# Kernel tuning notes

Hardware: AMD Instinct MI355X
Metric: run time of the kernel (lower is better)

Reference implementation:

```python
import jax, jax.numpy as jnp
import numpy as np
from jax import lax

B, T, R = 64, 32, 49
LOCAL, QVEC, EMB, HID, VOCAB = 1024, 512, 256, 512, 10000
START_IDX = 1


def setup_inputs() -> dict:
    key = jax.random.key(0)
    ks = jax.random.split(key, 20)
    s = lambda k, shape, scale=0.02: jax.random.normal(k, shape, dtype=jnp.float32) * scale
    return {
        "image_local_features": jax.random.normal(ks[0], (B, R, LOCAL), dtype=jnp.float32),
        "image_global_features": jax.random.normal(ks[1], (B, 2 * LOCAL), dtype=jnp.float32),
        "question_vectors": jax.random.normal(ks[2], (B, QVEC), dtype=jnp.float32),
        "answers": jax.random.randint(ks[3], (B, T), 0, VOCAB),
        "emb": s(ks[4], (VOCAB, EMB), 1.0),
        "W_g2o": s(ks[5], (HID, 2 * LOCAL)),
        "b_g2o": jnp.zeros((HID,), jnp.float32),
        "W_h": s(ks[6], (HID, QVEC)),
        "W_c": s(ks[7], (HID, QVEC)),
        "W_ih": s(ks[8], (4 * HID, EMB + HID)),
        "W_hh": s(ks[9], (4 * HID, HID)),
        "b_ih": jnp.zeros((4 * HID,), jnp.float32),
        "b_hh": jnp.zeros((4 * HID,), jnp.float32),
        "W_attn": s(ks[10], (HID, LOCAL)),
        "W_u": s(ks[11], (HID, LOCAL + HID)),
        "b_u": jnp.zeros((HID,), jnp.float32),
        "W_vocab": s(ks[12], (VOCAB, HID)),
        "b_vocab": jnp.zeros((VOCAB,), jnp.float32),
    }


def reference(image_local_features, image_global_features, question_vectors, answers,
              emb, W_g2o, b_g2o, W_h, W_c, W_ih, W_hh, b_ih, b_hh,
              W_attn, W_u, b_u, W_vocab, b_vocab):
    batch, max_len = answers.shape
    # initial decoder inputs / states
    y0 = jnp.broadcast_to(emb[START_IDX], (batch, emb.shape[1]))          # [B,E]
    o0 = image_global_features @ W_g2o.T + b_g2o                          # [B,H]
    h0 = question_vectors @ W_h.T                                         # [B,H]
    c0 = question_vectors @ W_c.T                                         # [B,H]
    # teacher forcing: input at step t is answers[t-1] (start token at t=0)
    ans_emb = emb[answers]                                                # [B,T,E]
    y_seq = jnp.concatenate([y0[:, None, :], ans_emb[:, :-1, :]], axis=1) # [B,T,E]
    y_seq = jnp.swapaxes(y_seq, 0, 1)                                     # [T,B,E]
    # precompute attention projection of local features (loop-invariant)
    attn_proj = jnp.einsum('brf,hf->brh', image_local_features, W_attn)   # [B,R,H]

    def step(carry, y_t):
        h, c, o = carry
        x = jnp.concatenate([y_t, o], axis=1)                             # [B,E+H]
        gates = x @ W_ih.T + b_ih + h @ W_hh.T + b_hh                     # [B,4H]
        i_g, f_g, g_g, o_g = jnp.split(gates, 4, axis=1)
        c = jax.nn.sigmoid(f_g) * c + jax.nn.sigmoid(i_g) * jnp.tanh(g_g)
        h = jax.nn.sigmoid(o_g) * jnp.tanh(c)
        e = jnp.einsum('brh,bh->br', attn_proj, h)                        # [B,R]
        att = jax.nn.softmax(e, axis=-1)
        a = jnp.einsum('brf,br->bf', image_local_features, att)           # [B,F]
        u = jnp.concatenate([a, h], axis=1)                               # [B,F+H]
        o = jnp.tanh(u @ W_u.T + b_u)                                     # dropout_prob=0 -> identity
        logits = o @ W_vocab.T + b_vocab                                  # [B,V]
        return (h, c, o), logits

    _, logits = lax.scan(step, (h0, c0, o0), y_seq)                       # [T,B,V]
    return jnp.swapaxes(logits, 0, 1)                                     # [B,T,V]
```

## Files before the change

### kernel.cpp

```cpp
#include <hip/hip_runtime.h>

#define DI __device__ __forceinline__

typedef float f32x4 __attribute__((ext_vector_type(4)));
typedef __bf16 bf16x8 __attribute__((ext_vector_type(8)));
typedef __bf16 bf16x4 __attribute__((ext_vector_type(4)));

static DI f32x4 mfma_bf16(bf16x8 a, bf16x8 b, f32x4 c) {
    return __builtin_amdgcn_mfma_f32_16x16x32_bf16(a, b, c, 0, 0, 0);
}
static DI bf16x8 ldb8(const __bf16* p) { return *(const bf16x8*)p; }
static DI float sigf(float x) { return 1.0f / (1.0f + expf(-x)); }

static DI void stc_u32(void* p, unsigned v) {
    __hip_atomic_store((unsigned*)p, v, __ATOMIC_RELAXED, __HIP_MEMORY_SCOPE_AGENT);
}
static DI void stc_u64(void* p, unsigned long long v) {
    __hip_atomic_store((unsigned long long*)p, v, __ATOMIC_RELAXED, __HIP_MEMORY_SCOPE_AGENT);
}
static DI unsigned ldc_u32(const void* p) {
    return __hip_atomic_load((const unsigned*)p, __ATOMIC_RELAXED, __HIP_MEMORY_SCOPE_AGENT);
}

#define GRID_BLKS 64

static DI void garrive(unsigned* F, int blk, unsigned tgt) {
    __syncthreads();
    if (threadIdx.x == 0)
        __hip_atomic_store(&F[blk], tgt, __ATOMIC_RELAXED, __HIP_MEMORY_SCOPE_AGENT);
}
static DI void gwait_all(unsigned* F, unsigned tgt) {
    if (threadIdx.x < 64) {
        for (;;) {
            unsigned f = __hip_atomic_load(&F[threadIdx.x], __ATOMIC_RELAXED,
                                           __HIP_MEMORY_SCOPE_AGENT);
            if (__all(f >= tgt)) break;
            __builtin_amdgcn_s_sleep(1);
        }
    }
    __syncthreads();
}

__global__ void convert_kernel(
    const float* Wih, const float* Whh,
    const float* bih, const float* bhh, const float* Wu,
    const float* emb, const int* answers,
    __bf16* WGo, float* biasg, __bf16* WhTo, __bf16* Yo)
{
    int z = blockIdx.z;
    int stride = gridDim.x * blockDim.x;
    int tid0 = blockIdx.x * blockDim.x + threadIdx.x;
    if (z == 0) {
        const int N = 2048 * 1280;
        for (int i = tid0; i < N; i += stride) {
            int n = i / 1280, k = i - n * 1280;
            int r = (n & 3) * 512 + (n >> 2);
            float val = (k < 768) ? Wih[r * 768 + k] : Whh[r * 512 + (k - 768)];
            WGo[i] = (__bf16)val;
        }
        for (int n = tid0; n < 2048; n += stride) {
            int r = (n & 3) * 512 + (n >> 2);
            biasg[n] = bih[r] + bhh[r];
        }
    } else if (z == 1) {
        const int N = 512 * 512;
        for (int i = tid0; i < N; i += stride) {
            int k = i >> 9, u = i & 511;
            WhTo[i] = (__bf16)Wu[(size_t)u * 1536 + 1024 + k];
        }
    } else {
        const int N = 32 * 64 * 256;
        for (int i = tid0; i < N; i += stride) {
            int t = i >> 14;
            int b = (i >> 8) & 63;
            int e = i & 255;
            int tok = (t == 0) ? 1 : answers[b * 32 + (t - 1)];
            Yo[i] = (__bf16)emb[tok * 256 + e];
        }
    }
}

__global__ void init_kernel(
    const float* q, const float* g,
    const float* Wh, const float* Wc, const float* Wg2o, const float* bg2o,
    __bf16* h0b, float* c0f, __bf16* o0b)
{
    int z = blockIdx.z;
    const float* A; const float* B; int K;
    if (z == 0)      { A = q; B = Wh;   K = 512; }
    else if (z == 1) { A = q; B = Wc;   K = 512; }
    else             { A = g; B = Wg2o; K = 2048; }
    int n0 = blockIdx.x * 64, m0 = blockIdx.y * 16;
    __shared__ float As[32][16];
    __shared__ float Bs[32][64];
    int tid = threadIdx.x;
    int n = tid & 63, tyq = tid >> 6;
    float acc[4] = {0.f, 0.f, 0.f, 0.f};
    for (int k0 = 0; k0 < K; k0 += 32) {
        {
            int idx = tid * 2, row = idx >> 5, kk = idx & 31;
            const float* ar = A + (m0 + row) * K + k0 + kk;
            As[kk][row] = ar[0];
            As[kk + 1][row] = ar[1];
        }
        {
            int row = tid >> 2, kk = (tid & 3) * 8;
            const float* br = B + (n0 + row) * K + k0 + kk;
            float4 v0 = *(const float4*)br;
            float4 v1 = *(const float4*)(br + 4);
            Bs[kk + 0][row] = v0.x; Bs[kk + 1][row] = v0.y;
            Bs[kk + 2][row] = v0.z; Bs[kk + 3][row] = v0.w;
            Bs[kk + 4][row] = v1.x; Bs[kk + 5][row] = v1.y;
            Bs[kk + 6][row] = v1.z; Bs[kk + 7][row] = v1.w;
        }
        __syncthreads();
        #pragma unroll
        for (int k = 0; k < 32; k++) {
            float4 a = *(const float4*)&As[k][tyq * 4];
            float b = Bs[k][n];
            acc[0] += a.x * b; acc[1] += a.y * b; acc[2] += a.z * b; acc[3] += a.w * b;
        }
        __syncthreads();
    }
    int ng = n0 + n;
    #pragma unroll
    for (int i = 0; i < 4; i++) {
        int m = m0 + tyq * 4 + i;
        float v = acc[i];
        if (z == 0)      { h0b[m * 512 + ng] = (__bf16)v; }
        else if (z == 1) { c0f[m * 512 + ng] = v; }
        else             { o0b[m * 512 + ng] = (__bf16)(v + bg2o[ng]); }
    }
}

__global__ __launch_bounds__(256) void attnproj_kernel(
    const float* Af, const float* Bf, int ldb, __bf16* APo)
{
    __shared__ __bf16 As[64][72];
    __shared__ __bf16 Bs[64][72];
    int tid = threadIdx.x;
    int m0 = blockIdx.x * 64, n0 = blockIdx.y * 64;
    int w = tid >> 6, lane = tid & 63, row16 = lane & 15, kg = lane >> 4;
    f32x4 acc[4] = {};
    for (int k0 = 0; k0 < 1024; k0 += 64) {
        int r = tid >> 2, col = (tid & 3) * 16;
        const float* ap = Af + (size_t)(m0 + r) * 1024 + k0 + col;
        const float* bp = Bf + (size_t)(n0 + r) * ldb + k0 + col;
        bf16x8 va0, va1, vb0, vb1;
        #pragma unroll
        for (int u = 0; u < 8; u++) {
            va0[u] = (__bf16)ap[u]; va1[u] = (__bf16)ap[u + 8];
            vb0[u] = (__bf16)bp[u]; vb1[u] = (__bf16)bp[u + 8];
        }
        *(bf16x8*)&As[r][col] = va0; *(bf16x8*)&As[r][col + 8] = va1;
        *(bf16x8*)&Bs[r][col] = vb0; *(bf16x8*)&Bs[r][col + 8] = vb1;
        __syncthreads();
        #pragma unroll
        for (int kt = 0; kt < 2; kt++) {
            bf16x8 af = *(const bf16x8*)&As[w * 16 + row16][kt * 32 + kg * 8];
            #pragma unroll
            for (int j = 0; j < 4; j++) {
                bf16x8 bfv = *(const bf16x8*)&Bs[j * 16 + row16][kt * 32 + kg * 8];
                acc[j] = mfma_bf16(af, bfv, acc[j]);
            }
        }
        __syncthreads();
    }
    #pragma unroll
    for (int j = 0; j < 4; j++)
        #pragma unroll
        for (int r = 0; r < 4; r++)
            APo[(size_t)(m0 + w * 16 + kg * 4 + r) * 512 + n0 + j * 16 + row16] =
                (__bf16)acc[j][r];
}

__global__ __launch_bounds__(256, 1) void loop_kernel(
    const __bf16* Yall, const __bf16* WG, const float* BG,
    const __bf16* WhT, const float* bu,
    const __bf16* APb, const __bf16* LUb, const float* CF0,
    __bf16* OS, __bf16* HS, __bf16* CHP, unsigned* FLA, unsigned* FLB)
{
    __shared__ float S[64][34];
    __shared__ float Cs[64][8];
    __shared__ float Hs[64][8];
    __shared__ __bf16 Ws[8][512];
    __shared__ __bf16 WGs[32 * 1280];
    __shared__ float BGs[32];
    __shared__ float esh[64];
    __shared__ float ash[64];
    int tid = threadIdx.x;
    int blk = blockIdx.x;
    int w = tid >> 6, lane = tid & 63, row16 = lane & 15, kg4 = lane >> 4;
    int n0 = blk * 32;

    for (int i = tid; i < 32 * 160; i += 256) {
        int n = i / 160, g = i % 160;
        bf16x8 v = ldb8(WG + (size_t)(n0 + n) * 1280 + g * 8);
        *(bf16x8*)((char*)WGs + ((n * 2560 + g * 16) ^ ((n & 7) << 4))) = v;
    }
    for (int i = tid; i < 8 * 512; i += 256)
        Ws[i >> 9][i & 511] = WhT[(size_t)(blk * 8 + (i >> 9)) * 512 + (i & 511)];
    if (tid < 32) BGs[tid] = BG[n0 + tid];
    {
        int b = tid >> 2, u0 = (tid & 3) * 2;
        Cs[b][u0]     = CF0[b * 512 + blk * 8 + u0];
        Cs[b][u0 + 1] = CF0[b * 512 + blk * 8 + u0 + 1];
    }
    __syncthreads();
    float wreg[8][4];
    {
        int u0c = (tid & 127) * 4;
        #pragma unroll
        for (int k = 0; k < 8; k++)
            #pragma unroll
            for (int j = 0; j < 4; j++)
                wreg[k][j] = (float)Ws[k][u0c + j];
    }

    for (int t = 0; t < 32; t++) {
        int arow = w * 16 + row16;
        f32x4 acc[2] = {};
        {
            const __bf16* Yt = Yall + t * 16384;
            const __bf16* Hp = HS + t * 32768;
            bf16x8 a_h[16];
            #pragma unroll
            for (int kt = 0; kt < 16; kt++)
                a_h[kt] = ldb8(Hp + arow * 512 + kt * 32 + kg4 * 8);
            asm volatile("" ::: "memory");
            #pragma unroll
            for (int kt = 0; kt < 8; kt++) {
                bf16x8 af = ldb8(Yt + arow * 256 + kt * 32 + kg4 * 8);
                #pragma unroll
                for (int nt = 0; nt < 2; nt++) {
                    int row = nt * 16 + row16;
                    bf16x8 bfv = *(const bf16x8*)((const char*)WGs +
                        ((row * 2560 + kt * 64 + kg4 * 16) ^ ((row & 7) << 4)));
                    acc[nt] = mfma_bf16(af, bfv, acc[nt]);
                }
            }
            #pragma unroll
            for (int kt = 24; kt < 40; kt++) {
                bf16x8 af = a_h[kt - 24];
                #pragma unroll
                for (int nt = 0; nt < 2; nt++) {
                    int row = nt * 16 + row16;
                    bf16x8 bfv = *(const bf16x8*)((const char*)WGs +
                        ((row * 2560 + kt * 64 + kg4 * 16) ^ ((row & 7) << 4)));
                    acc[nt] = mfma_bf16(af, bfv, acc[nt]);
                }
            }
        }
        gwait_all(FLB, (unsigned)t);

        {
            const __bf16* Op = OS + t * 32768;
            bf16x8 a_o[16];
            #pragma unroll
            for (int kt = 0; kt < 16; kt++)
                a_o[kt] = ldb8(Op + arow * 512 + kt * 32 + kg4 * 8);
            asm volatile("" ::: "memory");
            #pragma unroll
            for (int kt = 8; kt < 24; kt++) {
                bf16x8 af = a_o[kt - 8];
                #pragma unroll
                for (int nt = 0; nt < 2; nt++) {
                    int row = nt * 16 + row16;
                    bf16x8 bfv = *(const bf16x8*)((const char*)WGs +
                        ((row * 2560 + kt * 64 + kg4 * 16) ^ ((row & 7) << 4)));
                    acc[nt] = mfma_bf16(af, bfv, acc[nt]);
                }
            }
            #pragma unroll
            for (int nt = 0; nt < 2; nt++)
                #pragma unroll
                for (int r = 0; r < 4; r++)
                    S[w * 16 + kg4 * 4 + r][nt * 16 + row16] = acc[nt][r];
            __syncthreads();
            {
                int b = tid >> 2, u0 = (tid & 3) * 2;
                float h2[2];
                #pragma unroll
                for (int uu = 0; uu < 2; uu++) {
                    int u = u0 + uu;
                    float gi = S[b][u * 4 + 0] + BGs[u * 4 + 0];
                    float gf = S[b][u * 4 + 1] + BGs[u * 4 + 1];
                    float gg = S[b][u * 4 + 2] + BGs[u * 4 + 2];
                    float go = S[b][u * 4 + 3] + BGs[u * 4 + 3];
                    float cp = Cs[b][u];
                    float cn = sigf(gf) * cp + sigf(gi) * tanhf(gg);
                    h2[uu] = sigf(go) * tanhf(cn);
                    Cs[b][u] = cn;
                }
                Hs[b][u0] = h2[0];
                Hs[b][u0 + 1] = h2[1];
                union { __bf16 h[2]; unsigned v; } pk;
                pk.h[0] = (__bf16)h2[0]; pk.h[1] = (__bf16)h2[1];
                stc_u32((unsigned*)(HS + (t + 1) * 32768 + b * 512 + blk * 8 + u0), pk.v);
            }
            __syncthreads();
            {
                __bf16* CHPt = CHP + (size_t)(t & 1) * 2097152;
                int bh = tid >> 7;
                int u0 = (tid & 127) * 4;
                #pragma unroll 4
                for (int bb = 0; bb < 32; bb++) {
                    int b = bh * 32 + bb;
                    float4 hv0 = *(const float4*)&Hs[b][0];
                    float4 hv1 = *(const float4*)&Hs[b][4];
                    float a0 = 0.f, a1 = 0.f, a2 = 0.f, a3 = 0.f;
                    a0 += hv0.x * wreg[0][0]; a1 += hv0.x * wreg[0][1];
                    a2 += hv0.x * wreg[0][2]; a3 += hv0.x * wreg[0][3];
                    a0 += hv0.y * wreg[1][0]; a1 += hv0.y * wreg[1][1];
                    a2 += hv0.y * wreg[1][2]; a3 += hv0.y * wreg[1][3];
                    a0 += hv0.z * wreg[2][0]; a1 += hv0.z * wreg[2][1];
                    a2 += hv0.z * wreg[2][2]; a3 += hv0.z * wreg[2][3];
                    a0 += hv0.w * wreg[3][0]; a1 += hv0.w * wreg[3][1];
                    a2 += hv0.w * wreg[3][2]; a3 += hv0.w * wreg[3][3];
                    a0 += hv1.x * wreg[4][0]; a1 += hv1.x * wreg[4][1];
                    a2 += hv1.x * wreg[4][2]; a3 += hv1.x * wreg[4][3];
                    a0 += hv1.y * wreg[5][0]; a1 += hv1.y * wreg[5][1];
                    a2 += hv1.y * wreg[5][2]; a3 += hv1.y * wreg[5][3];
                    a0 += hv1.z * wreg[6][0]; a1 += hv1.z * wreg[6][1];
                    a2 += hv1.z * wreg[6][2]; a3 += hv1.z * wreg[6][3];
                    a0 += hv1.w * wreg[7][0]; a1 += hv1.w * wreg[7][1];
                    a2 += hv1.w * wreg[7][2]; a3 += hv1.w * wreg[7][3];
                    union { __bf16 h[4]; unsigned long long q; } pk;
                    pk.h[0] = (__bf16)a0; pk.h[1] = (__bf16)a1;
                    pk.h[2] = (__bf16)a2; pk.h[3] = (__bf16)a3;
                    stc_u64(CHPt + ((size_t)blk * 64 + b) * 512 + u0, pk.q);
                }
            }
        }
        garrive(FLA, blk, (unsigned)(t + 1));
        gwait_all(FLA, (unsigned)(t + 1));

        {
            int b = blk;
            const __bf16* hb = HS + (size_t)(t + 1) * 32768 + b * 512;
            const __bf16* CHPt = CHP + (size_t)(t & 1) * 2097152;
            bf16x8 h8 = ldb8(hb + lane * 8);
            unsigned cv[64];
            {
                const __bf16* cp = CHPt + (size_t)b * 512 + tid * 2;
                #pragma unroll
                for (int p = 0; p < 64; p++)
                    cv[p] = ldc_u32(cp + (size_t)p * 32768);
            }
            asm volatile("" ::: "memory");
            for (int r = w; r < 49; r += 4) {
                bf16x8 ap8 = ldb8(APb + (size_t)(b * 49 + r) * 512 + lane * 8);
                float s = 0.f;
                #pragma unroll
                for (int u = 0; u < 8; u++) s += (float)ap8[u] * (float)h8[u];
                #pragma unroll
                for (int off = 32; off > 0; off >>= 1) s += __shfl_xor(s, off);
                if (lane == 0) esh[r] = s;
            }
            __syncthreads();
            if (tid < 64) {
                float v = (tid < 49) ? esh[tid] : -3.0e38f;
                float mx = v;
                #pragma unroll
                for (int off = 32; off > 0; off >>= 1) mx = fmaxf(mx, __shfl_xor(mx, off));
                float ex = (tid < 49) ? expf(v - mx) : 0.0f;
                float sm = ex;
                #pragma unroll
                for (int off = 32; off > 0; off >>= 1) sm += __shfl_xor(sm, off);
                if (tid < 49) ash[tid] = ex / sm;
            }
            float oh0, oh1;
            {
                float s00 = 0.f, s01 = 0.f, s10 = 0.f, s11 = 0.f;
                float s20 = 0.f, s21 = 0.f, s30 = 0.f, s31 = 0.f;
                #pragma unroll
                for (int p = 0; p < 64; p += 4) {
                    union { unsigned u; __bf16 h[2]; } c0, c1, c2, c3;
                    c0.u = cv[p]; c1.u = cv[p + 1]; c2.u = cv[p + 2]; c3.u = cv[p + 3];
                    s00 += (float)c0.h[0]; s01 += (float)c0.h[1];
                    s10 += (float)c1.h[0]; s11 += (float)c1.h[1];
                    s20 += (float)c2.h[0]; s21 += (float)c2.h[1];
                    s30 += (float)c3.h[0]; s31 += (float)c3.h[1];
                }
                oh0 = (s00 + s10) + (s20 + s30);
                oh1 = (s01 + s11) + (s21 + s31);
            }
            __syncthreads();
            float oa0 = 0.f, oa1 = 0.f, ob0 = 0.f, ob1 = 0.f;
            {
                const __bf16* lu = LUb + (size_t)b * 49 * 512 + tid * 2;
                #pragma unroll 8
                for (int r = 0; r < 48; r += 2) {
                    float wt0 = ash[r], wt1 = ash[r + 1];
                    union { unsigned u; __bf16 h[2]; } c0, c1;
                    c0.u = *(const unsigned*)(lu + (size_t)r * 512);
                    c1.u = *(const unsigned*)(lu + (size_t)(r + 1) * 512);
                    oa0 += wt0 * (float)c0.h[0]; oa1 += wt0 * (float)c0.h[1];
                    ob0 += wt1 * (float)c1.h[0]; ob1 += wt1 * (float)c1.h[1];
                }
                float wt = ash[48];
                union { unsigned u; __bf16 h[2]; } c;
                c.u = *(const unsigned*)(lu + (size_t)48 * 512);
                oa0 += wt * (float)c.h[0]; oa1 += wt * (float)c.h[1];
                oa0 += ob0; oa1 += ob1;
            }
            int u = tid * 2;
            float o0v = tanhf(oh0 + oa0 + bu[u]);
            float o1v = tanhf(oh1 + oa1 + bu[u + 1]);
            union { __bf16 h[2]; unsigned v; } pk;
            pk.h[0] = (__bf16)o0v; pk.h[1] = (__bf16)o1v;
            stc_u32((unsigned*)(OS + (size_t)(t + 1) * 32768 + b * 512 + u), pk.v);
        }
        garrive(FLB, blk, (unsigned)(t + 1));
    }
}

__global__ __launch_bounds__(256) void vocab_kernel(
    const __bf16* A, const float* Wv, const float* bv, float* out)
{
    __shared__ __bf16 As[128][72];
    __shared__ __bf16 Bs[128][72];
    int tid = threadIdx.x;
    int m0 = blockIdx.x * 128;
    int n0 = blockIdx.y * 128;
    int w = tid >> 6, lane = tid & 63, row16 = lane & 15, kg = lane >> 4;
    int mw = (w & 1) * 64, nw = (w >> 1) * 64;
    f32x4 acc[4][4] = {};
    for (int k0 = 0; k0 < 512; k0 += 64) {
        #pragma unroll
        for (int q = 0; q < 2; q++) {
            int c = q * 256 + tid;
            int r = c >> 2, col = (c & 3) * 16;
            bf16x8 v0 = ldb8(A + (size_t)(m0 + r) * 512 + k0 + col);
            bf16x8 v1 = ldb8(A + (size_t)(m0 + r) * 512 + k0 + col + 8);
            *(bf16x8*)&As[r][col] = v0;
            *(bf16x8*)&As[r][col + 8] = v1;
            bf16x8 u0, u1;
            int nrow = n0 + r;
            if (nrow < 10000) {
                const float* bp = Wv + (size_t)nrow * 512 + k0 + col;
                #pragma unroll
                for (int u = 0; u < 8; u++) {
                    u0[u] = (__bf16)bp[u];
                    u1[u] = (__bf16)bp[u + 8];
                }
            } else {
                u0 = (bf16x8)(__bf16)0.0f;
                u1 = (bf16x8)(__bf16)0.0f;
            }
            *(bf16x8*)&Bs[r][col] = u0;
            *(bf16x8*)&Bs[r][col + 8] = u1;
        }
        __syncthreads();
        #pragma unroll
        for (int kt = 0; kt < 2; kt++) {
            bf16x8 af[4], bfr[4];
            #pragma unroll
            for (int i = 0; i < 4; i++)
                af[i] = *(const bf16x8*)&As[mw + i * 16 + row16][kt * 32 + kg * 8];
            #pragma unroll
            for (int j = 0; j < 4; j++)
                bfr[j] = *(const bf16x8*)&Bs[nw + j * 16 + row16][kt * 32 + kg * 8];
            #pragma unroll
            for (int i = 0; i < 4; i++)
                #pragma unroll
                for (int j = 0; j < 4; j++)
                    acc[i][j] = mfma_bf16(af[i], bfr[j], acc[i][j]);
        }
        __syncthreads();
    }
    #pragma unroll
    for (int j = 0; j < 4; j++) {
        int n = n0 + nw + j * 16 + row16;
        if (n < 10000) {
            float bvn = bv[n];
            #pragma unroll
            for (int i = 0; i < 4; i++) {
                #pragma unroll
                for (int r = 0; r < 4; r++) {
                    int m = m0 + mw + i * 16 + kg * 4 + r;
                    int tt = m >> 6, b = m & 63;
                    out[(size_t)(b * 32 + tt) * 10000 + n] = acc[i][j][r] + bvn;
                }
            }
        }
    }
}

extern "C" void kernel_launch(void* const* d_in, const int* in_sizes, int n_in,
                              void* d_out, int out_size, void* d_ws, size_t ws_size,
                              hipStream_t stream) {
    (void)in_sizes; (void)n_in; (void)out_size; (void)ws_size;
    const float* localf  = (const float*)d_in[0];
    const float* globalf = (const float*)d_in[1];
    const float* qvec    = (const float*)d_in[2];
    const int*   answers = (const int*)d_in[3];
    const float* emb     = (const float*)d_in[4];
    const float* Wg2o    = (const float*)d_in[5];
    const float* bg2o    = (const float*)d_in[6];
    const float* Wh      = (const float*)d_in[7];
    const float* Wc      = (const float*)d_in[8];
    const float* Wih     = (const float*)d_in[9];
    const float* Whh     = (const float*)d_in[10];
    const float* bih     = (const float*)d_in[11];
    const float* bhh     = (const float*)d_in[12];
    const float* Wattn   = (const float*)d_in[13];
    const float* Wu      = (const float*)d_in[14];
    const float* bu      = (const float*)d_in[15];
    const float* Wvocab  = (const float*)d_in[16];
    const float* bvocab  = (const float*)d_in[17];
    float* out = (float*)d_out;

    char* ws = (char*)d_ws;
    __bf16* WG  = (__bf16*)(ws + 0);
    __bf16* WhT = (__bf16*)(ws + 5242880);
    __bf16* Y   = (__bf16*)(ws + 5767168);
    float*  BG  = (float*) (ws + 6815744);
    __bf16* OS  = (__bf16*)(ws + 6823936);
    __bf16* HS  = (__bf16*)(ws + 8986624);
    float*  CF0 = (float*) (ws + 11149312);
    __bf16* APb = (__bf16*)(ws + 11280384);
    __bf16* LUb = (__bf16*)(ws + 14491648);
    __bf16* CHP = (__bf16*)(ws + 17702912);
    unsigned* FLA = (unsigned*)(ws + 26091520);
    unsigned* FLB = (unsigned*)(ws + 26091776);

    hipMemsetAsync(FLA, 0, 512, stream);
    convert_kernel<<<dim3(1024, 1, 3), 256, 0, stream>>>(
        Wih, Whh, bih, bhh, Wu, emb, answers,
        WG, BG, WhT, Y);
    init_kernel<<<dim3(8, 4, 3), 256, 0, stream>>>(
        qvec, globalf, Wh, Wc, Wg2o, bg2o, HS, CF0, OS);
    attnproj_kernel<<<dim3(49, 8), 256, 0, stream>>>(localf, Wattn, 1024, APb);
    attnproj_kernel<<<dim3(49, 8), 256, 0, stream>>>(localf, Wu, 1536, LUb);
    loop_kernel<<<GRID_BLKS, 256, 0, stream>>>(
        Y, WG, BG, WhT, bu, APb, LUb, CF0, OS, HS, CHP, FLA, FLB);
    vocab_kernel<<<dim3(16, 79), 256, 0, stream>>>(OS + 32768, Wvocab, bvocab, out);
}
```

Measured before the change: 1.123 ms.

## Split recurrent loop into LSTM and attention block roles, stage weights in LDS

The persistent loop kernel now launches 128 blocks. Blocks 0-63 compute the LSTM gates and blocks 64-127 each handle one batch row's attention and output projection, handing off through the FLA/FLB flags. The per-batch attention projection and local-feature tables are now cached in shared memory rather than reread from global memory every step. The vocab GEMM is restructured so each block converts one 128-row slice of W_vocab to bf16 once and reuses it across 8 M tiles, and the weight conversion kernel now walks rows. This cuts the per-step global barrier into a producer/consumer pipeline and avoids repeated fp32 weight conversion, at the cost of more LDS per block and more flag polling.

```diff
diff --git a/kernel.cpp b/kernel.cpp
--- a/kernel.cpp
+++ b/kernel.cpp
@@ -22,12 +22,11 @@
     return __hip_atomic_load((const unsigned*)p, __ATOMIC_RELAXED, __HIP_MEMORY_SCOPE_AGENT);
 }
 
-#define GRID_BLKS 64
-
-static DI void garrive(unsigned* F, int blk, unsigned tgt) {
+
+static DI void garrive(unsigned* F, int idx, unsigned tgt) {
     __syncthreads();
     if (threadIdx.x == 0)
-        __hip_atomic_store(&F[blk], tgt, __ATOMIC_RELAXED, __HIP_MEMORY_SCOPE_AGENT);
+        __hip_atomic_store(&F[idx], tgt, __ATOMIC_RELAXED, __HIP_MEMORY_SCOPE_AGENT);
 }
 static DI void gwait_all(unsigned* F, unsigned tgt) {
     if (threadIdx.x < 64) {
@@ -51,14 +50,18 @@
     int stride = gridDim.x * blockDim.x;
     int tid0 = blockIdx.x * blockDim.x + threadIdx.x;
     if (z == 0) {
-        const int N = 2048 * 1280;
-        for (int i = tid0; i < N; i += stride) {
-            int n = i / 1280, k = i - n * 1280;
+        #pragma unroll
+        for (int rr = 0; rr < 2; rr++) {
+            int n = blockIdx.x * 2 + rr;
             int r = (n & 3) * 512 + (n >> 2);
-            float val = (k < 768) ? Wih[r * 768 + k] : Whh[r * 512 + (k - 768)];
-            WGo[i] = (__bf16)val;
-        }
-        for (int n = tid0; n < 2048; n += stride) {
+            const float* sih = Wih + (size_t)r * 768;
+            const float* shh = Whh + (size_t)r * 512;
+            __bf16* dst = WGo + (size_t)n * 1280;
+            for (int k = threadIdx.x; k < 1280; k += 256)
+                dst[k] = (__bf16)((k < 768) ? sih[k] : shh[k - 768]);
+        }
+        if (blockIdx.x < 8) {
+            int n = blockIdx.x * 256 + threadIdx.x;
             int r = (n & 3) * 512 + (n >> 2);
             biasg[n] = bih[r] + bhh[r];
         }
@@ -185,158 +188,172 @@
     __shared__ float Hs[64][8];
     __shared__ __bf16 Ws[8][512];
     __shared__ __bf16 WGs[32 * 1280];
+    __shared__ __bf16 LUs[49 * 512];
     __shared__ float BGs[32];
     __shared__ float esh[64];
     __shared__ float ash[64];
     int tid = threadIdx.x;
     int blk = blockIdx.x;
     int w = tid >> 6, lane = tid & 63, row16 = lane & 15, kg4 = lane >> 4;
-    int n0 = blk * 32;
-
-    for (int i = tid; i < 32 * 160; i += 256) {
-        int n = i / 160, g = i % 160;
-        bf16x8 v = ldb8(WG + (size_t)(n0 + n) * 1280 + g * 8);
-        *(bf16x8*)((char*)WGs + ((n * 2560 + g * 16) ^ ((n & 7) << 4))) = v;
-    }
-    for (int i = tid; i < 8 * 512; i += 256)
-        Ws[i >> 9][i & 511] = WhT[(size_t)(blk * 8 + (i >> 9)) * 512 + (i & 511)];
-    if (tid < 32) BGs[tid] = BG[n0 + tid];
-    {
-        int b = tid >> 2, u0 = (tid & 3) * 2;
-        Cs[b][u0]     = CF0[b * 512 + blk * 8 + u0];
-        Cs[b][u0 + 1] = CF0[b * 512 + blk * 8 + u0 + 1];
-    }
-    __syncthreads();
-    float wreg[8][4];
-    {
-        int u0c = (tid & 127) * 4;
-        #pragma unroll
-        for (int k = 0; k < 8; k++)
+
+    if (blk < 64) {
+        int n0 = blk * 32;
+        for (int i = tid; i < 32 * 160; i += 256) {
+            int n = i / 160, g = i % 160;
+            bf16x8 v = ldb8(WG + (size_t)(n0 + n) * 1280 + g * 8);
+            *(bf16x8*)((char*)WGs + ((n * 2560 + g * 16) ^ ((n & 7) << 4))) = v;
+        }
+        for (int i = tid; i < 8 * 512; i += 256)
+            Ws[i >> 9][i & 511] = WhT[(size_t)(blk * 8 + (i >> 9)) * 512 + (i & 511)];
+        if (tid < 32) BGs[tid] = BG[n0 + tid];
+        {
+            int b = tid >> 2, u0 = (tid & 3) * 2;
+            Cs[b][u0]     = CF0[b * 512 + blk * 8 + u0];
+            Cs[b][u0 + 1] = CF0[b * 512 + blk * 8 + u0 + 1];
+        }
+        __syncthreads();
+        float wreg[8][4];
+        {
+            int u0c = (tid & 127) * 4;
             #pragma unroll
-            for (int j = 0; j < 4; j++)
-                wreg[k][j] = (float)Ws[k][u0c + j];
-    }
-
-    for (int t = 0; t < 32; t++) {
-        int arow = w * 16 + row16;
-        f32x4 acc[2] = {};
+            for (int k = 0; k < 8; k++)
+                #pragma unroll
+                for (int j = 0; j < 4; j++)
+                    wreg[k][j] = (float)Ws[k][u0c + j];
+        }
+
+        for (int t = 0; t < 32; t++) {
+            gwait_all(FLA, (unsigned)t);
+            int arow = w * 16 + row16;
+            f32x4 acc[2] = {};
+            {
+                const __bf16* Yt = Yall + t * 16384;
+                const __bf16* Hp = HS + t * 32768;
+                bf16x8 a_h[16];
+                #pragma unroll
+                for (int kt = 0; kt < 16; kt++)
+                    a_h[kt] = ldb8(Hp + arow * 512 + kt * 32 + kg4 * 8);
+                asm volatile("" ::: "memory");
+                #pragma unroll
+                for (int kt = 0; kt < 8; kt++) {
+                    bf16x8 af = ldb8(Yt + arow * 256 + kt * 32 + kg4 * 8);
+                    #pragma unroll
+                    for (int nt = 0; nt < 2; nt++) {
+                        int row = nt * 16 + row16;
+                        bf16x8 bfv = *(const bf16x8*)((const char*)WGs +
+                            ((row * 2560 + kt * 64 + kg4 * 16) ^ ((row & 7) << 4)));
+                        acc[nt] = mfma_bf16(af, bfv, acc[nt]);
+                    }
+                }
+                #pragma unroll
+                for (int kt = 24; kt < 40; kt++) {
+                    bf16x8 af = a_h[kt - 24];
+                    #pragma unroll
+                    for (int nt = 0; nt < 2; nt++) {
+                        int row = nt * 16 + row16;
+                        bf16x8 bfv = *(const bf16x8*)((const char*)WGs +
+                            ((row * 2560 + kt * 64 + kg4 * 16) ^ ((row & 7) << 4)));
+                        acc[nt] = mfma_bf16(af, bfv, acc[nt]);
+                    }
+                }
+            }
+            gwait_all(FLB, (unsigned)t);
+            {
+                const __bf16* Op = OS + t * 32768;
+                bf16x8 a_o[16];
+                #pragma unroll
+                for (int kt = 0; kt < 16; kt++)
+                    a_o[kt] = ldb8(Op + arow * 512 + kt * 32 + kg4 * 8);
+                asm volatile("" ::: "memory");
+                #pragma unroll
+                for (int kt = 8; kt < 24; kt++) {
+                    bf16x8 af = a_o[kt - 8];
+                    #pragma unroll
+                    for (int nt = 0; nt < 2; nt++) {
+                        int row = nt * 16 + row16;
+                        bf16x8 bfv = *(const bf16x8*)((const char*)WGs +
+                            ((row * 2560 + kt * 64 + kg4 * 16) ^ ((row & 7) << 4)));
+                        acc[nt] = mfma_bf16(af, bfv, acc[nt]);
+                    }
+                }
+                #pragma unroll
+                for (int nt = 0; nt < 2; nt++)
+                    #pragma unroll
+                    for (int r = 0; r < 4; r++)
+                        S[w * 16 + kg4 * 4 + r][nt * 16 + row16] = acc[nt][r];
+                __syncthreads();
+                {
+                    int b = tid >> 2, u0 = (tid & 3) * 2;
+                    float h2[2];
+                    #pragma unroll
+                    for (int uu = 0; uu < 2; uu++) {
+                        int u = u0 + uu;
+                        float gi = S[b][u * 4 + 0] + BGs[u * 4 + 0];
+                        float gf = S[b][u * 4 + 1] + BGs[u * 4 + 1];
+                        float gg = S[b][u * 4 + 2] + BGs[u * 4 + 2];
+                        float go = S[b][u * 4 + 3] + BGs[u * 4 + 3];
+                        float cp = Cs[b][u];
+                        float cn = sigf(gf) * cp + sigf(gi) * tanhf(gg);
+                        h2[uu] = sigf(go) * tanhf(cn);
+                        Cs[b][u] = cn;
+                    }
+                    Hs[b][u0] = h2[0];
+                    Hs[b][u0 + 1] = h2[1];
+                    union { __bf16 h[2]; unsigned v; } pk;
+                    pk.h[0] = (__bf16)h2[0]; pk.h[1] = (__bf16)h2[1];
+                    stc_u32((unsigned*)(HS + (t + 1) * 32768 + b * 512 + blk * 8 + u0), pk.v);
+                }
+                __syncthreads();
+                {
+                    __bf16* CHPt = CHP + (size_t)(t & 1) * 2097152;
+                    int bh = tid >> 7;
+                    int u0 = (tid & 127) * 4;
+                    #pragma unroll 4
+                    for (int bb = 0; bb < 32; bb++) {
+                        int b = bh * 32 + bb;
+                        float4 hv0 = *(const float4*)&Hs[b][0];
+                        float4 hv1 = *(const float4*)&Hs[b][4];
+                        float a0 = 0.f, a1 = 0.f, a2 = 0.f, a3 = 0.f;
+                        a0 += hv0.x * wreg[0][0]; a1 += hv0.x * wreg[0][1];
+                        a2 += hv0.x * wreg[0][2]; a3 += hv0.x * wreg[0][3];
+                        a0 += hv0.y * wreg[1][0]; a1 += hv0.y * wreg[1][1];
+                        a2 += hv0.y * wreg[1][2]; a3 += hv0.y * wreg[1][3];
+                        a0 += hv0.z * wreg[2][0]; a1 += hv0.z * wreg[2][1];
+                        a2 += hv0.z * wreg[2][2]; a3 += hv0.z * wreg[2][3];
+                        a0 += hv0.w * wreg[3][0]; a1 += hv0.w * wreg[3][1];
+                        a2 += hv0.w * wreg[3][2]; a3 += hv0.w * wreg[3][3];
+                        a0 += hv1.x * wreg[4][0]; a1 += hv1.x * wreg[4][1];
+                        a2 += hv1.x * wreg[4][2]; a3 += hv1.x * wreg[4][3];
+                        a0 += hv1.y * wreg[5][0]; a1 += hv1.y * wreg[5][1];
+                        a2 += hv1.y * wreg[5][2]; a3 += hv1.y * wreg[5][3];
+                        a0 += hv1.z * wreg[6][0]; a1 += hv1.z * wreg[6][1];
+                        a2 += hv1.z * wreg[6][2]; a3 += hv1.z * wreg[6][3];
+                        a0 += hv1.w * wreg[7][0]; a1 += hv1.w * wreg[7][1];
+                        a2 += hv1.w * wreg[7][2]; a3 += hv1.w * wreg[7][3];
+                        union { __bf16 h[4]; unsigned long long q; } pk;
+                        pk.h[0] = (__bf16)a0; pk.h[1] = (__bf16)a1;
+                        pk.h[2] = (__bf16)a2; pk.h[3] = (__bf16)a3;
+                        stc_u64(CHPt + ((size_t)blk * 64 + b) * 512 + u0, pk.q);
+                    }
+                }
+            }
+            garrive(FLA, blk, (unsigned)(t + 1));
+        }
+    } else {
+        int b = blk - 64;
+        __bf16* APs = WGs;
         {
-            const __bf16* Yt = Yall + t * 16384;
-            const __bf16* Hp = HS + t * 32768;
-            bf16x8 a_h[16];
-            #pragma unroll
-            for (int kt = 0; kt < 16; kt++)
-                a_h[kt] = ldb8(Hp + arow * 512 + kt * 32 + kg4 * 8);
-            asm volatile("" ::: "memory");
-            #pragma unroll
-            for (int kt = 0; kt < 8; kt++) {
-                bf16x8 af = ldb8(Yt + arow * 256 + kt * 32 + kg4 * 8);
-                #pragma unroll
-                for (int nt = 0; nt < 2; nt++) {
-                    int row = nt * 16 + row16;
-                    bf16x8 bfv = *(const bf16x8*)((const char*)WGs +
-                        ((row * 2560 + kt * 64 + kg4 * 16) ^ ((row & 7) << 4)));
-                    acc[nt] = mfma_bf16(af, bfv, acc[nt]);
-                }
-            }
-            #pragma unroll
-            for (int kt = 24; kt < 40; kt++) {
-                bf16x8 af = a_h[kt - 24];
-                #pragma unroll
-                for (int nt = 0; nt < 2; nt++) {
-                    int row = nt * 16 + row16;
-                    bf16x8 bfv = *(const bf16x8*)((const char*)WGs +
-                        ((row * 2560 + kt * 64 + kg4 * 16) ^ ((row & 7) << 4)));
-                    acc[nt] = mfma_bf16(af, bfv, acc[nt]);
-                }
-            }
-        }
-        gwait_all(FLB, (unsigned)t);
-
-        {
-            const __bf16* Op = OS + t * 32768;
-            bf16x8 a_o[16];
-            #pragma unroll
-            for (int kt = 0; kt < 16; kt++)
-                a_o[kt] = ldb8(Op + arow * 512 + kt * 32 + kg4 * 8);
-            asm volatile("" ::: "memory");
-            #pragma unroll
-            for (int kt = 8; kt < 24; kt++) {
-                bf16x8 af = a_o[kt - 8];
-                #pragma unroll
-                for (int nt = 0; nt < 2; nt++) {
-                    int row = nt * 16 + row16;
-                    bf16x8 bfv = *(const bf16x8*)((const char*)WGs +
-                        ((row * 2560 + kt * 64 + kg4 * 16) ^ ((row & 7) << 4)));
-                    acc[nt] = mfma_bf16(af, bfv, acc[nt]);
-                }
-            }
-            #pragma unroll
-            for (int nt = 0; nt < 2; nt++)
-                #pragma unroll
-                for (int r = 0; r < 4; r++)
-                    S[w * 16 + kg4 * 4 + r][nt * 16 + row16] = acc[nt][r];
-            __syncthreads();
-            {
-                int b = tid >> 2, u0 = (tid & 3) * 2;
-                float h2[2];
-                #pragma unroll
-                for (int uu = 0; uu < 2; uu++) {
-                    int u = u0 + uu;
-                    float gi = S[b][u * 4 + 0] + BGs[u * 4 + 0];
-                    float gf = S[b][u * 4 + 1] + BGs[u * 4 + 1];
-                    float gg = S[b][u * 4 + 2] + BGs[u * 4 + 2];
-                    float go = S[b][u * 4 + 3] + BGs[u * 4 + 3];
-                    float cp = Cs[b][u];
-                    float cn = sigf(gf) * cp + sigf(gi) * tanhf(gg);
-                    h2[uu] = sigf(go) * tanhf(cn);
-                    Cs[b][u] = cn;
-                }
-                Hs[b][u0] = h2[0];
-                Hs[b][u0 + 1] = h2[1];
-                union { __bf16 h[2]; unsigned v; } pk;
-                pk.h[0] = (__bf16)h2[0]; pk.h[1] = (__bf16)h2[1];
-                stc_u32((unsigned*)(HS + (t + 1) * 32768 + b * 512 + blk * 8 + u0), pk.v);
-            }
-            __syncthreads();
-            {
-                __bf16* CHPt = CHP + (size_t)(t & 1) * 2097152;
-                int bh = tid >> 7;
-                int u0 = (tid & 127) * 4;
-                #pragma unroll 4
-                for (int bb = 0; bb < 32; bb++) {
-                    int b = bh * 32 + bb;
-                    float4 hv0 = *(const float4*)&Hs[b][0];
-                    float4 hv1 = *(const float4*)&Hs[b][4];
-                    float a0 = 0.f, a1 = 0.f, a2 = 0.f, a3 = 0.f;
-                    a0 += hv0.x * wreg[0][0]; a1 += hv0.x * wreg[0][1];
-                    a2 += hv0.x * wreg[0][2]; a3 += hv0.x * wreg[0][3];
-                    a0 += hv0.y * wreg[1][0]; a1 += hv0.y * wreg[1][1];
-                    a2 += hv0.y * wreg[1][2]; a3 += hv0.y * wreg[1][3];
-                    a0 += hv0.z * wreg[2][0]; a1 += hv0.z * wreg[2][1];
-                    a2 += hv0.z * wreg[2][2]; a3 += hv0.z * wreg[2][3];
-                    a0 += hv0.w * wreg[3][0]; a1 += hv0.w * wreg[3][1];
-                    a2 += hv0.w * wreg[3][2]; a3 += hv0.w * wreg[3][3];
-                    a0 += hv1.x * wreg[4][0]; a1 += hv1.x * wreg[4][1];
-                    a2 += hv1.x * wreg[4][2]; a3 += hv1.x * wreg[4][3];
-                    a0 += hv1.y * wreg[5][0]; a1 += hv1.y * wreg[5][1];
-                    a2 += hv1.y * wreg[5][2]; a3 += hv1.y * wreg[5][3];
-                    a0 += hv1.z * wreg[6][0]; a1 += hv1.z * wreg[6][1];
-                    a2 += hv1.z * wreg[6][2]; a3 += hv1.z * wreg[6][3];
-                    a0 += hv1.w * wreg[7][0]; a1 += hv1.w * wreg[7][1];
-                    a2 += hv1.w * wreg[7][2]; a3 += hv1.w * wreg[7][3];
-                    union { __bf16 h[4]; unsigned long long q; } pk;
-                    pk.h[0] = (__bf16)a0; pk.h[1] = (__bf16)a1;
-                    pk.h[2] = (__bf16)a2; pk.h[3] = (__bf16)a3;
-                    stc_u64(CHPt + ((size_t)blk * 64 + b) * 512 + u0, pk.q);
-                }
-            }
-        }
-        garrive(FLA, blk, (unsigned)(t + 1));
-        gwait_all(FLA, (unsigned)(t + 1));
-
-        {
-            int b = blk;
+            const bf16x8* src_ap = (const bf16x8*)(APb + (size_t)b * 49 * 512);
+            const bf16x8* src_lu = (const bf16x8*)(LUb + (size_t)b * 49 * 512);
+            for (int i = tid; i < 49 * 64; i += 256) {
+                ((bf16x8*)APs)[i] = src_ap[i];
+                ((bf16x8*)LUs)[i] = src_lu[i];
+            }
+        }
+        __syncthreads();
+
+        for (int t = 0; t < 32; t++) {
+            gwait_all(FLA, (unsigned)(t + 1));
             const __bf16* hb = HS + (size_t)(t + 1) * 32768 + b * 512;
             const __bf16* CHPt = CHP + (size_t)(t & 1) * 2097152;
             bf16x8 h8 = ldb8(hb + lane * 8);
@@ -349,7 +366,7 @@
             }
             asm volatile("" ::: "memory");
             for (int r = w; r < 49; r += 4) {
-                bf16x8 ap8 = ldb8(APb + (size_t)(b * 49 + r) * 512 + lane * 8);
+                bf16x8 ap8 = *(const bf16x8*)&APs[r * 512 + lane * 8];
                 float s = 0.f;
                 #pragma unroll
                 for (int u = 0; u < 8; u++) s += (float)ap8[u] * (float)h8[u];
@@ -388,19 +405,19 @@
             __syncthreads();
             float oa0 = 0.f, oa1 = 0.f, ob0 = 0.f, ob1 = 0.f;
             {
-                const __bf16* lu = LUb + (size_t)b * 49 * 512 + tid * 2;
+                const __bf16* lu = LUs + tid * 2;
                 #pragma unroll 8
                 for (int r = 0; r < 48; r += 2) {
                     float wt0 = ash[r], wt1 = ash[r + 1];
                     union { unsigned u; __bf16 h[2]; } c0, c1;
-                    c0.u = *(const unsigned*)(lu + (size_t)r * 512);
-                    c1.u = *(const unsigned*)(lu + (size_t)(r + 1) * 512);
+                    c0.u = *(const unsigned*)(lu + r * 512);
+                    c1.u = *(const unsigned*)(lu + (r + 1) * 512);
                     oa0 += wt0 * (float)c0.h[0]; oa1 += wt0 * (float)c0.h[1];
                     ob0 += wt1 * (float)c1.h[0]; ob1 += wt1 * (float)c1.h[1];
                 }
                 float wt = ash[48];
                 union { unsigned u; __bf16 h[2]; } c;
-                c.u = *(const unsigned*)(lu + (size_t)48 * 512);
+                c.u = *(const unsigned*)(lu + 48 * 512);
                 oa0 += wt * (float)c.h[0]; oa1 += wt * (float)c.h[1];
                 oa0 += ob0; oa1 += ob1;
             }
@@ -410,77 +427,80 @@
             union { __bf16 h[2]; unsigned v; } pk;
             pk.h[0] = (__bf16)o0v; pk.h[1] = (__bf16)o1v;
             stc_u32((unsigned*)(OS + (size_t)(t + 1) * 32768 + b * 512 + u), pk.v);
-        }
-        garrive(FLB, blk, (unsigned)(t + 1));
+            garrive(FLB, b, (unsigned)(t + 1));
+        }
     }
 }
 
 __global__ __launch_bounds__(256) void vocab_kernel(
     const __bf16* A, const float* Wv, const float* bv, float* out)
 {
+    __shared__ __bf16 Bs[128][520];
     __shared__ __bf16 As[128][72];
-    __shared__ __bf16 Bs[128][72];
     int tid = threadIdx.x;
-    int m0 = blockIdx.x * 128;
-    int n0 = blockIdx.y * 128;
+    int n0 = blockIdx.x * 128;
+    int m00 = blockIdx.y * 1024;
     int w = tid >> 6, lane = tid & 63, row16 = lane & 15, kg = lane >> 4;
     int mw = (w & 1) * 64, nw = (w >> 1) * 64;
-    f32x4 acc[4][4] = {};
-    for (int k0 = 0; k0 < 512; k0 += 64) {
+    {
+        int r = tid >> 1, half = tid & 1;
+        int nrow = n0 + r;
+        int c0 = half * 256;
+        if (nrow < 10000) {
+            const float* bp = Wv + (size_t)nrow * 512 + c0;
+            for (int c = 0; c < 256; c += 8) {
+                bf16x8 v;
+                #pragma unroll
+                for (int u = 0; u < 8; u++) v[u] = (__bf16)bp[c + u];
+                *(bf16x8*)&Bs[r][c0 + c] = v;
+            }
+        } else {
+            bf16x8 z = (bf16x8)(__bf16)0.0f;
+            for (int c = 0; c < 256; c += 8) *(bf16x8*)&Bs[r][c0 + c] = z;
+        }
+    }
+    __syncthreads();
+    for (int mt = 0; mt < 8; mt++) {
+        int m0 = m00 + mt * 128;
+        f32x4 acc[4][4] = {};
+        for (int k0 = 0; k0 < 512; k0 += 64) {
+            #pragma unroll
+            for (int q = 0; q < 4; q++) {
+                int idx = q * 256 + tid;
+                int r = idx >> 3, col = (idx & 7) * 8;
+                *(bf16x8*)&As[r][col] = ldb8(A + (size_t)(m0 + r) * 512 + k0 + col);
+            }
+            __syncthreads();
+            #pragma unroll
+            for (int kt = 0; kt < 2; kt++) {
+                bf16x8 af[4], bfr[4];
+                #pragma unroll
+                for (int i = 0; i < 4; i++)
+                    af[i] = *(const bf16x8*)&As[mw + i * 16 + row16][kt * 32 + kg * 8];
+                #pragma unroll
+                for (int j = 0; j < 4; j++)
+                    bfr[j] = *(const bf16x8*)&Bs[nw + j * 16 + row16][k0 + kt * 32 + kg * 8];
+                #pragma unroll
+                for (int i = 0; i < 4; i++)
+                    #pragma unroll
+                    for (int j = 0; j < 4; j++)
+                        acc[i][j] = mfma_bf16(af[i], bfr[j], acc[i][j]);
+            }
+            __syncthreads();
+        }
         #pragma unroll
-        for (int q = 0; q < 2; q++) {
-            int c = q * 256 + tid;
-            int r = c >> 2, col = (c & 3) * 16;
-            bf16x8 v0 = ldb8(A + (size_t)(m0 + r) * 512 + k0 + col);
-            bf16x8 v1 = ldb8(A + (size_t)(m0 + r) * 512 + k0 + col + 8);
-            *(bf16x8*)&As[r][col] = v0;
-            *(bf16x8*)&As[r][col + 8] = v1;
-            bf16x8 u0, u1;
-            int nrow = n0 + r;
-            if (nrow < 10000) {
-                const float* bp = Wv + (size_t)nrow * 512 + k0 + col;
-                #pragma unroll
-                for (int u = 0; u < 8; u++) {
-                    u0[u] = (__bf16)bp[u];
-                    u1[u] = (__bf16)bp[u + 8];
-                }
-            } else {
-                u0 = (bf16x8)(__bf16)0.0f;
-                u1 = (bf16x8)(__bf16)0.0f;
-            }
-            *(bf16x8*)&Bs[r][col] = u0;
-            *(bf16x8*)&Bs[r][col + 8] = u1;
-        }
-        __syncthreads();
-        #pragma unroll
-        for (int kt = 0; kt < 2; kt++) {
-            bf16x8 af[4], bfr[4];
-            #pragma unroll
-            for (int i = 0; i < 4; i++)
-                af[i] = *(const bf16x8*)&As[mw + i * 16 + row16][kt * 32 + kg * 8];
-            #pragma unroll
-            for (int j = 0; j < 4; j++)
-                bfr[j] = *(const bf16x8*)&Bs[nw + j * 16 + row16][kt * 32 + kg * 8];
-            #pragma unroll
-            for (int i = 0; i < 4; i++)
-                #pragma unroll
-                for (int j = 0; j < 4; j++)
-                    acc[i][j] = mfma_bf16(af[i], bfr[j], acc[i][j]);
-        }
-        __syncthreads();
-    }
-    #pragma unroll
-    for (int j = 0; j < 4; j++) {
-        int n = n0 + nw + j * 16 + row16;
-        if (n < 10000) {
-            float bvn = bv[n];
-            #pragma unroll
-            for (int i = 0; i < 4; i++) {
-                #pragma unroll
-                for (int r = 0; r < 4; r++) {
-                    int m = m0 + mw + i * 16 + kg * 4 + r;
-                    int tt = m >> 6, b = m & 63;
-                    out[(size_t)(b * 32 + tt) * 10000 + n] = acc[i][j][r] + bvn;
+        for (int j = 0; j < 4; j++) {
+            int n = n0 + nw + j * 16 + row16;
+            if (n < 10000) {
+                float bvn = bv[n];
+                #pragma unroll
+                for (int i = 0; i < 4; i++) {
+                    #pragma unroll
+                    for (int r = 0; r < 4; r++) {
+                        int m = m0 + mw + i * 16 + kg * 4 + r;
+                        int tt = m >> 6, b = m & 63;
+                        out[(size_t)(b * 32 + tt) * 10000 + n] = acc[i][j][r] + bvn;
+                    }
                 }
             }
         }
@@ -533,7 +553,7 @@
         qvec, globalf, Wh, Wc, Wg2o, bg2o, HS, CF0, OS);
     attnproj_kernel<<<dim3(49, 8), 256, 0, stream>>>(localf, Wattn, 1024, APb);
     attnproj_kernel<<<dim3(49, 8), 256, 0, stream>>>(localf, Wu, 1536, LUb);
-    loop_kernel<<<GRID_BLKS, 256, 0, stream>>>(
+    loop_kernel<<<128, 256, 0, stream>>>(
         Y, WG, BG, WhT, bu, APb, LUb, CF0, OS, HS, CHP, FLA, FLB);
-    vocab_kernel<<<dim3(16, 79), 256, 0, stream>>>(OS + 32768, Wvocab, bvocab, out);
-}
+    vocab_kernel<<<dim3(79, 2), 256, 0, stream>>>(OS + 32768, Wvocab, bvocab, out);
+}
```

New measurement: 962.8 us. -14.3%, faster.
